# Kernel optimization log

Measured on AMD Instinct MI355X. Metric: run time of the kernel, lower is better.

The kernel has to match this reference:

```python
import jax, jax.numpy as jnp
import numpy as np

N = 100000
E = 1600000
ROUND = 2


def spmm(src, dst, x):
    # adj.matmul(x) with binary sparse adjacency given as edge list:
    # out[dst] += x[src]
    return jax.ops.segment_sum(x[src], dst, num_segments=N)


def setup_inputs() -> dict:
    key = jax.random.key(0)
    ks = jax.random.split(key, 8)
    x = jax.random.normal(ks[0], (N, 512), dtype=jnp.float32)
    W_embed = jax.random.normal(ks[1], (512, 64), dtype=jnp.float32) * (1.0 / np.sqrt(512))
    b_embed = jnp.zeros((64,), dtype=jnp.float32)
    W_cls = jax.random.normal(ks[2], (448, 40), dtype=jnp.float32) * (1.0 / np.sqrt(448))
    b_cls = jnp.zeros((40,), dtype=jnp.float32)
    adj_src = jax.random.randint(ks[3], (E,), 0, N, dtype=jnp.int32)
    adj_dst = jax.random.randint(ks[4], (E,), 0, N, dtype=jnp.int32)
    adj2_src = jax.random.randint(ks[5], (E,), 0, N, dtype=jnp.int32)
    adj2_dst = jax.random.randint(ks[6], (E,), 0, N, dtype=jnp.int32)
    return {"x": x, "W_embed": W_embed, "b_embed": b_embed, "W_cls": W_cls,
            "b_cls": b_cls, "adj_src": adj_src, "adj_dst": adj_dst,
            "adj2_src": adj2_src, "adj2_dst": adj2_dst}


def reference(x, W_embed, b_embed, W_cls, b_cls, adj_src, adj_dst, adj2_src, adj2_dst):
    # embed: Linear + ReLU
    h = jax.nn.relu(x @ W_embed + b_embed)  # [N, 64]
    hidden_reps = [h]
    for _ in range(ROUND):
        r1 = spmm(adj_src, adj_dst, h)      # 1-hop aggregation
        r2 = spmm(adj2_src, adj2_dst, h)    # 2-hop aggregation
        h = jnp.concatenate([r1, r2], axis=-1)
        hidden_reps.append(h)
    hf = jnp.concatenate(hidden_reps, axis=-1)  # [N, 64*(2^(ROUND+1)-1)] = [N, 448]
    # dropout is identity in eval mode
    logits = hf @ W_cls + b_cls
    return jax.nn.log_softmax(logits, axis=1)
```

## Files before the change

### kernel.cpp

```cpp
#include <hip/hip_runtime.h>
#include <hip/hip_bf16.h>

#define NN 100000
#define EE 1600000
#define NBK 196
#define BSH 9
#define EPB 4096
#define STG 10240

using frag8 = __attribute__((ext_vector_type(8))) short;
using f32x4 = __attribute__((ext_vector_type(4))) float;

__device__ inline unsigned short f2bf(float f) {
    unsigned u = __float_as_uint(f);
    u = u + 0x7FFFu + ((u >> 16) & 1u);
    return (unsigned short)(u >> 16);
}
__device__ inline float bf2f(unsigned short u) {
    return __uint_as_float(((unsigned)u) << 16);
}
__device__ inline unsigned pack_bf16(float a, float b) {
    __hip_bfloat162 h = __float22bfloat162_rn(float2{a, b});
    union { __hip_bfloat162 h2; unsigned u; } c;
    c.h2 = h;
    return c.u;
}


__global__ __launch_bounds__(256) void bhist_k(const int* __restrict__ d1,
                                               const int* __restrict__ d2,
                                               int* __restrict__ bcnt) {
    __shared__ int lh[NBK];
    int adj = blockIdx.y;
    const int* dd = adj ? d2 : d1;
    int t = threadIdx.x;
    for (int i = t; i < NBK; i += 256) lh[i] = 0;
    __syncthreads();
    int e0 = blockIdx.x * EPB;
    #pragma unroll
    for (int k = 0; k < 16; ++k) {
        int e = e0 + k * 256 + t;
        if (e < EE) atomicAdd(&lh[dd[e] >> BSH], 1);
    }
    __syncthreads();
    for (int i = t; i < NBK; i += 256)
        if (lh[i]) atomicAdd(&bcnt[adj * NBK + i], lh[i]);
}

__global__ __launch_bounds__(256) void bscan_k(const int* __restrict__ bcnt,
                                               int* __restrict__ bbase,
                                               int* __restrict__ bcur) {
    int adj = blockIdx.x;
    __shared__ int s[256];
    int t = threadIdx.x;
    int v = (t < NBK) ? bcnt[adj * NBK + t] : 0;
    s[t] = v;
    __syncthreads();
    for (int off = 1; off < 256; off <<= 1) {
        int u = (t >= off) ? s[t - off] : 0;
        __syncthreads();
        s[t] += u;
        __syncthreads();
    }
    if (t < NBK) {
        int ex = s[t] - v;
        bbase[adj * (NBK + 1) + t] = ex;
        bcur[adj * NBK + t] = ex;
    }
    if (t == NBK - 1) bbase[adj * (NBK + 1) + NBK] = s[t];
}

__global__ __launch_bounds__(256) void binA_k(const int* __restrict__ s1,
                                              const int* __restrict__ d1,
                                              const int* __restrict__ s2,
                                              const int* __restrict__ d2,
                                              int* __restrict__ bcur,
                                              uint2* __restrict__ tmp1,
                                              uint2* __restrict__ tmp2) {
    __shared__ int lhist[NBK], lbase[NBK], gbase[NBK], lcur[NBK];
    __shared__ int sscan[256];
    __shared__ int stot;
    __shared__ uint2 stage[EPB];
    int adj = blockIdx.y;
    const int* ss = adj ? s2 : s1;
    const int* dd = adj ? d2 : d1;
    uint2* tmp = adj ? tmp2 : tmp1;
    int t = threadIdx.x;
    for (int i = t; i < NBK; i += 256) { lhist[i] = 0; lcur[i] = 0; }
    __syncthreads();
    int e0 = blockIdx.x * EPB;
    int d[16], s[16];
    #pragma unroll
    for (int k = 0; k < 16; ++k) {
        int e = e0 + k * 256 + t;
        d[k] = (e < EE) ? dd[e] : -1;
        s[k] = (e < EE) ? ss[e] : 0;
        if (d[k] >= 0) atomicAdd(&lhist[d[k] >> BSH], 1);
    }
    __syncthreads();
    int hv = (t < NBK) ? lhist[t] : 0;
    sscan[t] = hv;
    __syncthreads();
    for (int off = 1; off < 256; off <<= 1) {
        int u = (t >= off) ? sscan[t - off] : 0;
        __syncthreads();
        sscan[t] += u;
        __syncthreads();
    }
    if (t < NBK) lbase[t] = sscan[t] - hv;
    if (t == NBK - 1) stot = sscan[t];
    __syncthreads();
    for (int i = t; i < NBK; i += 256)
        gbase[i] = lhist[i] ? atomicAdd(&bcur[adj * NBK + i], lhist[i]) : 0;
    __syncthreads();
    #pragma unroll
    for (int k = 0; k < 16; ++k) {
        if (d[k] >= 0) {
            int b = d[k] >> BSH;
            int pos = lbase[b] + atomicAdd(&lcur[b], 1);
            stage[pos] = make_uint2((unsigned)d[k], (unsigned)s[k]);
        }
    }
    __syncthreads();
    int tot = stot;
    for (int i = t; i < tot; i += 256) {
        uint2 u = stage[i];
        int b = u.x >> BSH;
        tmp[gbase[b] + (i - lbase[b])] = u;
    }
}

__global__ __launch_bounds__(256) void binB_k(const uint2* __restrict__ tmp1,
                                              const uint2* __restrict__ tmp2,
                                              const int* __restrict__ bbase,
                                              int* __restrict__ rs1,
                                              int* __restrict__ rs2,
                                              int* __restrict__ csr1,
                                              int* __restrict__ csr2) {
    __shared__ int cnt[512], cur[512];
    __shared__ int sscan[256];
    __shared__ int stage[STG];
    int adj = blockIdx.y, b = blockIdx.x;
    const uint2* tmp = adj ? tmp2 : tmp1;
    int* rs  = adj ? rs2  : rs1;
    int* csr = adj ? csr2 : csr1;
    int t = threadIdx.x;
    int n0 = b << BSH;
    int n1 = n0 + 512; if (n1 > NN) n1 = NN;
    int nn = n1 - n0;
    int base = bbase[adj * (NBK + 1) + b];
    int count = bbase[adj * (NBK + 1) + b + 1] - base;
    cnt[t] = 0; cnt[t + 256] = 0;
    __syncthreads();
    for (int i = t; i < count; i += 256)
        atomicAdd(&cnt[tmp[base + i].x - n0], 1);
    __syncthreads();
    int c0 = cnt[2 * t], c1 = cnt[2 * t + 1];
    int ps = c0 + c1;
    sscan[t] = ps;
    __syncthreads();
    for (int off = 1; off < 256; off <<= 1) {
        int u = (t >= off) ? sscan[t - off] : 0;
        __syncthreads();
        sscan[t] += u;
        __syncthreads();
    }
    int pe = sscan[t] - ps;
    int e0x = pe, e1x = pe + c0;
    if (2 * t < nn)     rs[n0 + 2 * t]     = base + e0x;
    if (2 * t + 1 < nn) rs[n0 + 2 * t + 1] = base + e1x;
    cur[2 * t] = e0x; cur[2 * t + 1] = e1x;
    if (t == 0 && n1 == NN) rs[NN] = base + count;
    __syncthreads();
    for (int i = t; i < count; i += 256) {
        uint2 u = tmp[base + i];
        int loc = atomicAdd(&cur[u.x - n0], 1);
        if (loc < STG) stage[loc] = (int)u.y;
        else csr[base + loc] = (int)u.y;
    }
    __syncthreads();
    int m = count < STG ? count : STG;
    for (int i = t; i < m; i += 256) csr[base + i] = stage[i];
}


__global__ void wconv_k(const float* __restrict__ W, unsigned short* __restrict__ Wbf) {
    int id = blockIdx.x * 256 + threadIdx.x;
    if (id < 512 * 64) {
        int k = id >> 6, col = id & 63;
        int ch = k >> 3, el = k & 7;
        int cs = (ch & ~15) | ((ch & 15) ^ (col & 7));
        Wbf[col * 512 + cs * 8 + el] = f2bf(W[id]);
    }
}


__global__ void wcls_k(const float* __restrict__ Wc, unsigned short* __restrict__ Wbig) {
    int id = blockIdx.x * 256 + threadIdx.x;
    int k = id >> 7, col = id & 127;
    float v = 0.f;
    if (col < 40) v = Wc[k * 40 + col];
    else if (col < 80)  { if (k >= 64) v = Wc[(192 + k - 64) * 40 + (col - 40)]; }
    else if (col < 120) { if (k >= 64) v = Wc[(320 + k - 64) * 40 + (col - 80)]; }
    int ch = k >> 3, el = k & 7;
    int phys = (ch & ~7) | ((ch & 7) ^ (col & 7));
    Wbig[col * 192 + phys * 8 + el] = f2bf(v);
}


__global__ __launch_bounds__(256) void embed_k(const float* __restrict__ x,
                                               const unsigned short* __restrict__ Wbf,
                                               const float* __restrict__ bias,
                                               unsigned short* __restrict__ hcat) {
    __shared__ unsigned short sA[64 * 128];
    __shared__ unsigned short sW[64 * 128];
    int tid = threadIdx.x;
    int lane = tid & 63, wave = tid >> 6;
    int row0 = blockIdx.x * 64;
    f32x4 acc[4];
    #pragma unroll
    for (int n = 0; n < 4; n++) acc[n] = (f32x4){0.f, 0.f, 0.f, 0.f};

    int ccol = tid & 15;
    int rbase = tid >> 4;

    for (int kt = 0; kt < 4; ++kt) {
        #pragma unroll
        for (int rr = 0; rr < 4; ++rr) {
            int r = rbase + rr * 16;
            int grow = row0 + r;
            float v[8];
            if (grow < NN) {
                const float4* px = (const float4*)(x + (size_t)grow * 512 + kt * 128 + ccol * 8);
                float4 p0 = px[0], p1 = px[1];
                v[0] = p0.x; v[1] = p0.y; v[2] = p0.z; v[3] = p0.w;
                v[4] = p1.x; v[5] = p1.y; v[6] = p1.z; v[7] = p1.w;
            } else {
                #pragma unroll
                for (int i = 0; i < 8; i++) v[i] = 0.f;
            }
            unsigned uu[4];
            #pragma unroll
            for (int i = 0; i < 4; i++)
                uu[i] = pack_bf16(v[2 * i], v[2 * i + 1]);
            int cs = ccol ^ (r & 7);
            uint4 pk; pk.x = uu[0]; pk.y = uu[1]; pk.z = uu[2]; pk.w = uu[3];
            *(uint4*)&sA[(r * 16 + cs) * 8] = pk;
        }
        for (int q = tid; q < 1024; q += 256) {
            int col = q >> 4, c = q & 15;
            ((uint4*)sW)[q] = ((const uint4*)Wbf)[col * 64 + kt * 16 + c];
        }
        __syncthreads();
        #pragma unroll
        for (int kk = 0; kk < 4; ++kk) {
            int ar = wave * 16 + (lane & 15);
            int ac = (kk * 4 + (lane >> 4)) ^ (ar & 7);
            frag8 a = *(const frag8*)&sA[(ar * 16 + ac) * 8];
            #pragma unroll
            for (int n = 0; n < 4; n++) {
                int col = n * 16 + (lane & 15);
                int bc = (kk * 4 + (lane >> 4)) ^ (col & 7);
                frag8 b = *(const frag8*)&sW[(col * 16 + bc) * 8];
                acc[n] = __builtin_amdgcn_mfma_f32_16x16x32_bf16(a, b, acc[n], 0, 0, 0);
            }
        }
        __syncthreads();
    }
    #pragma unroll
    for (int n = 0; n < 4; n++) {
        int col = n * 16 + (lane & 15);
        float bv = bias[col];
        #pragma unroll
        for (int i = 0; i < 4; i++) {
            int r = row0 + wave * 16 + (lane >> 4) * 4 + i;
            if (r < NN) {
                float vv = acc[n][i] + bv;
                vv = vv > 0.f ? vv : 0.f;
                hcat[(size_t)r * 192 + col] = f2bf(vv);
            }
        }
    }
}


__device__ inline void gacc8(float* a, uint4 u) {
    a[0] += bf2f((unsigned short)(u.x & 0xffff));
    a[1] += bf2f((unsigned short)(u.x >> 16));
    a[2] += bf2f((unsigned short)(u.y & 0xffff));
    a[3] += bf2f((unsigned short)(u.y >> 16));
    a[4] += bf2f((unsigned short)(u.z & 0xffff));
    a[5] += bf2f((unsigned short)(u.z >> 16));
    a[6] += bf2f((unsigned short)(u.w & 0xffff));
    a[7] += bf2f((unsigned short)(u.w >> 16));
}


__global__ __launch_bounds__(256) void round1_k(unsigned short* hc,
                                                const int* __restrict__ rs1,
                                                const int* __restrict__ csr1,
                                                const int* __restrict__ rs2,
                                                const int* __restrict__ csr2) {
    int wave = threadIdx.x >> 6, lane = threadIdx.x & 63;
    int row = blockIdx.x * 4 + wave;
    int g = lane >> 3, gl = lane & 7;

    #pragma unroll
    for (int which = 0; which < 2; ++which) {
        const int* rs  = which ? rs2  : rs1;
        const int* csr = which ? csr2 : csr1;
        int s = rs[row], e = rs[row + 1];
        float a[8] = {0.f, 0.f, 0.f, 0.f, 0.f, 0.f, 0.f, 0.f};
        for (int t0 = s; t0 < e; t0 += 64) {
            int rem = e - t0;
            int idxv = 0;
            if (lane < rem) idxv = csr[t0 + lane];
            int cnt = rem < 64 ? rem : 64;
            int nq = (cnt + 7) >> 3;
            int q = 0;
            for (; q + 2 <= nq; q += 2) {
                int j0 = q * 8 + g, j1 = j0 + 8;
                int s0 = __shfl(idxv, j0);
                int s1 = __shfl(idxv, j1);
                uint4 u0 = *(const uint4*)(hc + (size_t)s0 * 192 + gl * 8);
                uint4 u1 = *(const uint4*)(hc + (size_t)s1 * 192 + gl * 8);
                if (j0 < cnt) gacc8(a, u0);
                if (j1 < cnt) gacc8(a, u1);
            }
            for (; q < nq; ++q) {
                int j0 = q * 8 + g;
                int s0 = __shfl(idxv, j0);
                uint4 u0 = *(const uint4*)(hc + (size_t)s0 * 192 + gl * 8);
                if (j0 < cnt) gacc8(a, u0);
            }
        }
        #pragma unroll
        for (int i = 0; i < 8; ++i) {
            a[i] += __shfl_xor(a[i], 8);
            a[i] += __shfl_xor(a[i], 16);
            a[i] += __shfl_xor(a[i], 32);
        }
        if (lane < 8) {
            uint4 o;
            o.x = pack_bf16(a[0], a[1]);
            o.y = pack_bf16(a[2], a[3]);
            o.z = pack_bf16(a[4], a[5]);
            o.w = pack_bf16(a[6], a[7]);
            *(uint4*)(hc + (size_t)row * 192 + 64 + which * 64 + lane * 8) = o;
        }
    }
}


__global__ __launch_bounds__(256) void gemm_k(const unsigned short* __restrict__ hcat,
                                              const unsigned short* __restrict__ Wbig,
                                              const float* __restrict__ bc,
                                              float* __restrict__ logits,
                                              unsigned short* __restrict__ zcat) {
    __shared__ unsigned short sA[64 * 64];
    __shared__ unsigned short sB[128 * 64];
    int tid = threadIdx.x;
    int lane = tid & 63, wave = tid >> 6;
    int row0 = blockIdx.x * 64;
    f32x4 acc[8];
    #pragma unroll
    for (int n = 0; n < 8; n++) acc[n] = (f32x4){0.f, 0.f, 0.f, 0.f};

    for (int kt = 0; kt < 3; ++kt) {
        #pragma unroll
        for (int q = tid; q < 512; q += 256) {
            int r = q >> 3, c = q & 7;
            int phys = c ^ (r & 7);
            ((uint4*)sA)[r * 8 + phys] = ((const uint4*)hcat)[(size_t)(row0 + r) * 24 + kt * 8 + c];
        }
        #pragma unroll
        for (int q = tid; q < 1024; q += 256) {
            int col = q >> 3, c = q & 7;
            ((uint4*)sB)[q] = ((const uint4*)Wbig)[col * 24 + kt * 8 + c];
        }
        __syncthreads();
        #pragma unroll
        for (int kk = 0; kk < 2; ++kk) {
            int ar = wave * 16 + (lane & 15);
            int ac = (kk * 4 + (lane >> 4)) ^ (ar & 7);
            frag8 a = *(const frag8*)&sA[(ar * 8 + ac) * 8];
            #pragma unroll
            for (int n = 0; n < 8; n++) {
                int col = n * 16 + (lane & 15);
                int bcc = (kk * 4 + (lane >> 4)) ^ (col & 7);
                frag8 b = *(const frag8*)&sB[(col * 8 + bcc) * 8];
                acc[n] = __builtin_amdgcn_mfma_f32_16x16x32_bf16(a, b, acc[n], 0, 0, 0);
            }
        }
        __syncthreads();
    }
    #pragma unroll
    for (int n = 0; n < 8; n++) {
        int col = n * 16 + (lane & 15);
        float bv = (col < 40) ? bc[col] : 0.f;
        #pragma unroll
        for (int i = 0; i < 4; i++) {
            int r = row0 + wave * 16 + (lane >> 4) * 4 + i;
            if (r < NN) {
                float vv = acc[n][i];
                if (col < 40) {
                    logits[(size_t)r * 40 + col] = vv + bv;
                } else if (col < 80) {
                    zcat[(size_t)r * 128 + (col - 40)] = f2bf(vv);
                } else if (col < 120) {
                    zcat[(size_t)r * 128 + 64 + (col - 80)] = f2bf(vv);
                }
            }
        }
    }
}


__global__ __launch_bounds__(256) void round2_k(const unsigned short* __restrict__ zc,
                                                const int* __restrict__ rs1,
                                                const int* __restrict__ csr1,
                                                const int* __restrict__ rs2,
                                                const int* __restrict__ csr2,
                                                float* __restrict__ logits) {
    int wave = threadIdx.x >> 6, lane = threadIdx.x & 63;
    int row = blockIdx.x * 4 + wave;
    int g = lane >> 3, gl = lane & 7;

    float a[8] = {0.f, 0.f, 0.f, 0.f, 0.f, 0.f, 0.f, 0.f};
    #pragma unroll
    for (int which = 0; which < 2; ++which) {
        const int* rs  = which ? rs2  : rs1;
        const int* csr = which ? csr2 : csr1;
        int s = rs[row], e = rs[row + 1];
        size_t zoff = which * 64 + gl * 8;
        for (int t0 = s; t0 < e; t0 += 64) {
            int rem = e - t0;
            int idxv = 0;
            if (lane < rem) idxv = csr[t0 + lane];
            int cnt = rem < 64 ? rem : 64;
            int nq = (cnt + 7) >> 3;
            int q = 0;
            for (; q + 2 <= nq; q += 2) {
                int j0 = q * 8 + g, j1 = j0 + 8;
                int s0 = __shfl(idxv, j0);
                int s1 = __shfl(idxv, j1);
                uint4 u0 = *(const uint4*)(zc + (size_t)s0 * 128 + zoff);
                uint4 u1 = *(const uint4*)(zc + (size_t)s1 * 128 + zoff);
                if (j0 < cnt) gacc8(a, u0);
                if (j1 < cnt) gacc8(a, u1);
            }
            for (; q < nq; ++q) {
                int j0 = q * 8 + g;
                int s0 = __shfl(idxv, j0);
                uint4 u0 = *(const uint4*)(zc + (size_t)s0 * 128 + zoff);
                if (j0 < cnt) gacc8(a, u0);
            }
        }
    }
    #pragma unroll
    for (int i = 0; i < 8; ++i) {
        a[i] += __shfl_xor(a[i], 8);
        a[i] += __shfl_xor(a[i], 16);
        a[i] += __shfl_xor(a[i], 32);
    }

    bool act = lane < 5;
    float v[8];
    if (act) {
        float4 b0 = *(const float4*)(logits + (size_t)row * 40 + lane * 8);
        float4 b1 = *(const float4*)(logits + (size_t)row * 40 + lane * 8 + 4);
        v[0] = b0.x + a[0]; v[1] = b0.y + a[1]; v[2] = b0.z + a[2]; v[3] = b0.w + a[3];
        v[4] = b1.x + a[4]; v[5] = b1.y + a[5]; v[6] = b1.z + a[6]; v[7] = b1.w + a[7];
    } else {
        #pragma unroll
        for (int i = 0; i < 8; ++i) v[i] = -1e30f;
    }
    float m = fmaxf(fmaxf(fmaxf(v[0], v[1]), fmaxf(v[2], v[3])),
                    fmaxf(fmaxf(v[4], v[5]), fmaxf(v[6], v[7])));
    m = fmaxf(m, __shfl_xor(m, 1));
    m = fmaxf(m, __shfl_xor(m, 2));
    m = fmaxf(m, __shfl_xor(m, 4));
    float es = 0.f;
    if (act) {
        #pragma unroll
        for (int i = 0; i < 8; ++i) es += __expf(v[i] - m);
    }
    es += __shfl_xor(es, 1);
    es += __shfl_xor(es, 2);
    es += __shfl_xor(es, 4);
    float ls = __logf(es);
    if (act) {
        float4 o0, o1;
        o0.x = v[0] - m - ls; o0.y = v[1] - m - ls; o0.z = v[2] - m - ls; o0.w = v[3] - m - ls;
        o1.x = v[4] - m - ls; o1.y = v[5] - m - ls; o1.z = v[6] - m - ls; o1.w = v[7] - m - ls;
        *(float4*)(logits + (size_t)row * 40 + lane * 8)     = o0;
        *(float4*)(logits + (size_t)row * 40 + lane * 8 + 4) = o1;
    }
}


extern "C" void kernel_launch(void* const* d_in, const int* in_sizes, int n_in,
                              void* d_out, int out_size, void* d_ws, size_t ws_size,
                              hipStream_t stream) {
    const float* x       = (const float*)d_in[0];
    const float* W_embed = (const float*)d_in[1];
    const float* b_embed = (const float*)d_in[2];
    const float* W_cls   = (const float*)d_in[3];
    const float* b_cls   = (const float*)d_in[4];
    const int* a1src = (const int*)d_in[5];
    const int* a1dst = (const int*)d_in[6];
    const int* a2src = (const int*)d_in[7];
    const int* a2dst = (const int*)d_in[8];

    float* logits = (float*)d_out;
    float* ws = (float*)d_ws;

    const size_t OFF_HCAT = 0;
    const size_t OFF_ZCAT = 9600000;
    const size_t OFF_RS1  = 16000000;
    const size_t OFF_RS2  = 16100004;
    const size_t OFF_BB   = 16200008;
    const size_t OFF_BC   = 16200402;
    const size_t OFF_BCNT = 16200794;
    const size_t OFF_CSR1 = 16201188;
    const size_t OFF_CSR2 = 17801188;
    const size_t OFF_WBF  = 19401188;
    const size_t OFF_WBIG = 19417572;

    unsigned short* hcat = (unsigned short*)(ws + OFF_HCAT);
    unsigned short* zcat = (unsigned short*)(ws + OFF_ZCAT);
    uint2* tmp1 = (uint2*)(ws + OFF_HCAT);
    uint2* tmp2 = tmp1 + EE;
    int* rs1   = (int*)(ws + OFF_RS1);
    int* rs2   = (int*)(ws + OFF_RS2);
    int* bbase = (int*)(ws + OFF_BB);
    int* bcur  = (int*)(ws + OFF_BC);
    int* bcnt  = (int*)(ws + OFF_BCNT);
    int* csr1  = (int*)(ws + OFF_CSR1);
    int* csr2  = (int*)(ws + OFF_CSR2);
    unsigned short* wbf  = (unsigned short*)(ws + OFF_WBF);
    unsigned short* wbig = (unsigned short*)(ws + OFF_WBIG);

    hipMemsetAsync(ws + OFF_BCNT, 0, 392 * 4, stream);

    const int NBA = (EE + EPB - 1) / EPB;

    bhist_k<<<dim3(NBA, 2), 256, 0, stream>>>(a1dst, a2dst, bcnt);
    bscan_k<<<2, 256, 0, stream>>>(bcnt, bbase, bcur);
    binA_k<<<dim3(NBA, 2), 256, 0, stream>>>(a1src, a1dst, a2src, a2dst, bcur, tmp1, tmp2);
    binB_k<<<dim3(NBK, 2), 256, 0, stream>>>(tmp1, tmp2, bbase, rs1, rs2, csr1, csr2);

    wconv_k<<<128, 256, 0, stream>>>(W_embed, wbf);
    wcls_k<<<96, 256, 0, stream>>>(W_cls, wbig);
    embed_k<<<(NN + 63) / 64, 256, 0, stream>>>(x, wbf, b_embed, hcat);

    round1_k<<<NN / 4, 256, 0, stream>>>(hcat, rs1, csr1, rs2, csr2);
    gemm_k<<<(NN + 63) / 64, 256, 0, stream>>>(hcat, wbig, b_cls, logits, zcat);
    round2_k<<<NN / 4, 256, 0, stream>>>(zcat, rs1, csr1, rs2, csr2, logits);
}
```

Baseline: 308.8 us.

## Fuse first-round gather into classifier GEMM and compact h0 to 64 columns

The first-round neighbor aggregation is merged into the classifier GEMM kernel: each block gathers its 64 rows' aggregates straight into shared memory next to the h0 tile and then runs the MFMA GEMM, so the 192-wide hcat no longer makes a round trip through global memory. h0 is now stored densely at 64 columns, which shrinks the gather footprint, and both gather loops are unrolled from 2 to 4 to keep more loads in flight. The cost is that round-1 parallelism drops from 25000 blocks of 4 rows to about 1563 blocks of 64 rows, each wave handling 16 rows in sequence, and shared memory per block grows.

New measurement: 383.3 us. 1.24x slower.

```diff
diff --git a/kernel.cpp b/kernel.cpp
--- a/kernel.cpp
+++ b/kernel.cpp
@@ -211,7 +211,7 @@
 __global__ __launch_bounds__(256) void embed_k(const float* __restrict__ x,
                                                const unsigned short* __restrict__ Wbf,
                                                const float* __restrict__ bias,
-                                               unsigned short* __restrict__ hcat) {
+                                               unsigned short* __restrict__ h0) {
     __shared__ unsigned short sA[64 * 128];
     __shared__ unsigned short sW[64 * 128];
     int tid = threadIdx.x;
@@ -277,7 +277,7 @@
             if (r < NN) {
                 float vv = acc[n][i] + bv;
                 vv = vv > 0.f ? vv : 0.f;
-                hcat[(size_t)r * 192 + col] = f2bf(vv);
+                h0[(size_t)r * 64 + col] = f2bf(vv);
             }
         }
     }
@@ -296,83 +296,91 @@
 }
 
 
-__global__ __launch_bounds__(256) void round1_k(unsigned short* hc,
+__global__ __launch_bounds__(256) void r1gemm_k(const unsigned short* __restrict__ h0,
                                                 const int* __restrict__ rs1,
                                                 const int* __restrict__ csr1,
                                                 const int* __restrict__ rs2,
-                                                const int* __restrict__ csr2) {
-    int wave = threadIdx.x >> 6, lane = threadIdx.x & 63;
-    int row = blockIdx.x * 4 + wave;
-    int g = lane >> 3, gl = lane & 7;
-
-    #pragma unroll
-    for (int which = 0; which < 2; ++which) {
-        const int* rs  = which ? rs2  : rs1;
-        const int* csr = which ? csr2 : csr1;
-        int s = rs[row], e = rs[row + 1];
-        float a[8] = {0.f, 0.f, 0.f, 0.f, 0.f, 0.f, 0.f, 0.f};
-        for (int t0 = s; t0 < e; t0 += 64) {
-            int rem = e - t0;
-            int idxv = 0;
-            if (lane < rem) idxv = csr[t0 + lane];
-            int cnt = rem < 64 ? rem : 64;
-            int nq = (cnt + 7) >> 3;
-            int q = 0;
-            for (; q + 2 <= nq; q += 2) {
-                int j0 = q * 8 + g, j1 = j0 + 8;
-                int s0 = __shfl(idxv, j0);
-                int s1 = __shfl(idxv, j1);
-                uint4 u0 = *(const uint4*)(hc + (size_t)s0 * 192 + gl * 8);
-                uint4 u1 = *(const uint4*)(hc + (size_t)s1 * 192 + gl * 8);
-                if (j0 < cnt) gacc8(a, u0);
-                if (j1 < cnt) gacc8(a, u1);
-            }
-            for (; q < nq; ++q) {
-                int j0 = q * 8 + g;
-                int s0 = __shfl(idxv, j0);
-                uint4 u0 = *(const uint4*)(hc + (size_t)s0 * 192 + gl * 8);
-                if (j0 < cnt) gacc8(a, u0);
-            }
-        }
-        #pragma unroll
-        for (int i = 0; i < 8; ++i) {
-            a[i] += __shfl_xor(a[i], 8);
-            a[i] += __shfl_xor(a[i], 16);
-            a[i] += __shfl_xor(a[i], 32);
-        }
-        if (lane < 8) {
-            uint4 o;
-            o.x = pack_bf16(a[0], a[1]);
-            o.y = pack_bf16(a[2], a[3]);
-            o.z = pack_bf16(a[4], a[5]);
-            o.w = pack_bf16(a[6], a[7]);
-            *(uint4*)(hc + (size_t)row * 192 + 64 + which * 64 + lane * 8) = o;
-        }
-    }
-}
-
-
-__global__ __launch_bounds__(256) void gemm_k(const unsigned short* __restrict__ hcat,
-                                              const unsigned short* __restrict__ Wbig,
-                                              const float* __restrict__ bc,
-                                              float* __restrict__ logits,
-                                              unsigned short* __restrict__ zcat) {
-    __shared__ unsigned short sA[64 * 64];
-    __shared__ unsigned short sB[128 * 64];
+                                                const int* __restrict__ csr2,
+                                                const unsigned short* __restrict__ Wbig,
+                                                const float* __restrict__ bc,
+                                                float* __restrict__ logits,
+                                                unsigned short* __restrict__ zcat) {
+    __shared__ unsigned short sA[64 * 24 * 8];
+    __shared__ unsigned short sB[128 * 8 * 8];
     int tid = threadIdx.x;
     int lane = tid & 63, wave = tid >> 6;
     int row0 = blockIdx.x * 64;
+    int g = lane >> 3, gl = lane & 7;
+
+    #pragma unroll
+    for (int q = tid; q < 512; q += 256) {
+        int r = q >> 3, c = q & 7;
+        int grow = row0 + r;
+        uint4 u = make_uint4(0, 0, 0, 0);
+        if (grow < NN) u = ((const uint4*)h0)[(size_t)grow * 8 + c];
+        ((uint4*)sA)[r * 24 + (c ^ (r & 7))] = u;
+    }
+
+    for (int rr = 0; rr < 16; ++rr) {
+        int r = wave * 16 + rr;
+        int row = row0 + r;
+        #pragma unroll
+        for (int which = 0; which < 2; ++which) {
+            const int* rs  = which ? rs2  : rs1;
+            const int* csr = which ? csr2 : csr1;
+            int s = 0, e = 0;
+            if (row < NN) { s = rs[row]; e = rs[row + 1]; }
+            float a[8] = {0.f, 0.f, 0.f, 0.f, 0.f, 0.f, 0.f, 0.f};
+            for (int t0 = s; t0 < e; t0 += 64) {
+                int rem = e - t0;
+                int idxv = 0;
+                if (lane < rem) idxv = csr[t0 + lane];
+                int cnt = rem < 64 ? rem : 64;
+                int nq = (cnt + 7) >> 3;
+                int q = 0;
+                for (; q + 4 <= nq; q += 4) {
+                    int j0 = q * 8 + g, j1 = j0 + 8, j2 = j0 + 16, j3 = j0 + 24;
+                    int s0 = __shfl(idxv, j0), s1 = __shfl(idxv, j1);
+                    int s2 = __shfl(idxv, j2), s3 = __shfl(idxv, j3);
+                    uint4 u0 = *(const uint4*)(h0 + (size_t)s0 * 64 + gl * 8);
+                    uint4 u1 = *(const uint4*)(h0 + (size_t)s1 * 64 + gl * 8);
+                    uint4 u2 = *(const uint4*)(h0 + (size_t)s2 * 64 + gl * 8);
+                    uint4 u3 = *(const uint4*)(h0 + (size_t)s3 * 64 + gl * 8);
+                    if (j0 < cnt) gacc8(a, u0);
+                    if (j1 < cnt) gacc8(a, u1);
+                    if (j2 < cnt) gacc8(a, u2);
+                    if (j3 < cnt) gacc8(a, u3);
+                }
+                for (; q < nq; ++q) {
+                    int j0 = q * 8 + g;
+                    int s0 = __shfl(idxv, j0);
+                    uint4 u0 = *(const uint4*)(h0 + (size_t)s0 * 64 + gl * 8);
+                    if (j0 < cnt) gacc8(a, u0);
+                }
+            }
+            #pragma unroll
+            for (int i = 0; i < 8; ++i) {
+                a[i] += __shfl_xor(a[i], 8);
+                a[i] += __shfl_xor(a[i], 16);
+                a[i] += __shfl_xor(a[i], 32);
+            }
+            if (lane < 8) {
+                uint4 o;
+                o.x = pack_bf16(a[0], a[1]);
+                o.y = pack_bf16(a[2], a[3]);
+                o.z = pack_bf16(a[4], a[5]);
+                o.w = pack_bf16(a[6], a[7]);
+                ((uint4*)sA)[r * 24 + (which + 1) * 8 + (lane ^ (r & 7))] = o;
+            }
+        }
+    }
+    __syncthreads();
+
     f32x4 acc[8];
     #pragma unroll
     for (int n = 0; n < 8; n++) acc[n] = (f32x4){0.f, 0.f, 0.f, 0.f};
 
     for (int kt = 0; kt < 3; ++kt) {
-        #pragma unroll
-        for (int q = tid; q < 512; q += 256) {
-            int r = q >> 3, c = q & 7;
-            int phys = c ^ (r & 7);
-            ((uint4*)sA)[r * 8 + phys] = ((const uint4*)hcat)[(size_t)(row0 + r) * 24 + kt * 8 + c];
-        }
         #pragma unroll
         for (int q = tid; q < 1024; q += 256) {
             int col = q >> 3, c = q & 7;
@@ -383,7 +391,7 @@
         for (int kk = 0; kk < 2; ++kk) {
             int ar = wave * 16 + (lane & 15);
             int ac = (kk * 4 + (lane >> 4)) ^ (ar & 7);
-            frag8 a = *(const frag8*)&sA[(ar * 8 + ac) * 8];
+            frag8 a = *(const frag8*)&sA[(ar * 24 + kt * 8 + ac) * 8];
             #pragma unroll
             for (int n = 0; n < 8; n++) {
                 int col = n * 16 + (lane & 15);
@@ -440,14 +448,18 @@
             int cnt = rem < 64 ? rem : 64;
             int nq = (cnt + 7) >> 3;
             int q = 0;
-            for (; q + 2 <= nq; q += 2) {
-                int j0 = q * 8 + g, j1 = j0 + 8;
-                int s0 = __shfl(idxv, j0);
-                int s1 = __shfl(idxv, j1);
+            for (; q + 4 <= nq; q += 4) {
+                int j0 = q * 8 + g, j1 = j0 + 8, j2 = j0 + 16, j3 = j0 + 24;
+                int s0 = __shfl(idxv, j0), s1 = __shfl(idxv, j1);
+                int s2 = __shfl(idxv, j2), s3 = __shfl(idxv, j3);
                 uint4 u0 = *(const uint4*)(zc + (size_t)s0 * 128 + zoff);
                 uint4 u1 = *(const uint4*)(zc + (size_t)s1 * 128 + zoff);
+                uint4 u2 = *(const uint4*)(zc + (size_t)s2 * 128 + zoff);
+                uint4 u3 = *(const uint4*)(zc + (size_t)s3 * 128 + zoff);
                 if (j0 < cnt) gacc8(a, u0);
                 if (j1 < cnt) gacc8(a, u1);
+                if (j2 < cnt) gacc8(a, u2);
+                if (j3 < cnt) gacc8(a, u3);
             }
             for (; q < nq; ++q) {
                 int j0 = q * 8 + g;
@@ -515,21 +527,21 @@
     float* logits = (float*)d_out;
     float* ws = (float*)d_ws;
 
-    const size_t OFF_HCAT = 0;
-    const size_t OFF_ZCAT = 9600000;
-    const size_t OFF_RS1  = 16000000;
-    const size_t OFF_RS2  = 16100004;
-    const size_t OFF_BB   = 16200008;
-    const size_t OFF_BC   = 16200402;
-    const size_t OFF_BCNT = 16200794;
-    const size_t OFF_CSR1 = 16201188;
-    const size_t OFF_CSR2 = 17801188;
-    const size_t OFF_WBF  = 19401188;
-    const size_t OFF_WBIG = 19417572;
-
-    unsigned short* hcat = (unsigned short*)(ws + OFF_HCAT);
-    unsigned short* zcat = (unsigned short*)(ws + OFF_ZCAT);
-    uint2* tmp1 = (uint2*)(ws + OFF_HCAT);
+    const size_t OFF_H0   = 0;
+    const size_t OFF_ZT   = 3200000;
+    const size_t OFF_RS1  = 9600000;
+    const size_t OFF_RS2  = 9700004;
+    const size_t OFF_BB   = 9800008;
+    const size_t OFF_BC   = 9800402;
+    const size_t OFF_BCNT = 9800794;
+    const size_t OFF_CSR1 = 9801188;
+    const size_t OFF_CSR2 = 11401188;
+    const size_t OFF_WBF  = 13001188;
+    const size_t OFF_WBIG = 13017572;
+
+    unsigned short* h0   = (unsigned short*)(ws + OFF_H0);
+    unsigned short* zcat = (unsigned short*)(ws + OFF_ZT);
+    uint2* tmp1 = (uint2*)(ws + OFF_ZT);
     uint2* tmp2 = tmp1 + EE;
     int* rs1   = (int*)(ws + OFF_RS1);
     int* rs2   = (int*)(ws + OFF_RS2);
@@ -552,9 +564,9 @@
 
     wconv_k<<<128, 256, 0, stream>>>(W_embed, wbf);
     wcls_k<<<96, 256, 0, stream>>>(W_cls, wbig);
-    embed_k<<<(NN + 63) / 64, 256, 0, stream>>>(x, wbf, b_embed, hcat);
-
-    round1_k<<<NN / 4, 256, 0, stream>>>(hcat, rs1, csr1, rs2, csr2);
-    gemm_k<<<(NN + 63) / 64, 256, 0, stream>>>(hcat, wbig, b_cls, logits, zcat);
+    embed_k<<<(NN + 63) / 64, 256, 0, stream>>>(x, wbf, b_embed, h0);
+
+    r1gemm_k<<<(NN + 63) / 64, 256, 0, stream>>>(h0, rs1, csr1, rs2, csr2,
+                                                 wbig, b_cls, logits, zcat);
     round2_k<<<NN / 4, 256, 0, stream>>>(zcat, rs1, csr1, rs2, csr2, logits);
 }
```
